# Kernel tuning notes

Hardware: AMD Instinct MI355X
Metric: run time of the kernel (lower is better)

Reference implementation:

```python
import jax, jax.numpy as jnp
import numpy as np

N_R = 100_000   # real nodes
N_E = 1_200_000 # r2r edges
G = 4096        # graphs (= interaction nodes, one per graph)
H = 64          # hidden_dim
ND = 64         # node_dim
ED = 16         # edge_dim
L = 4           # conv_layers
TGT = 1         # target_dim
SLOPE = 0.1     # LeakyReLU negative slope used by ISATconv


def _seg_softmax(logits, seg, n):
    m = jax.ops.segment_max(logits, seg, num_segments=n)
    ex = jnp.exp(logits - m[seg])
    s = jax.ops.segment_sum(ex, seg, num_segments=n)
    return ex / s[seg]


def setup_inputs() -> dict:
    key = jax.random.key(0)
    ks = jax.random.split(key, 20)
    inp = {}
    inp['r_node'] = jax.random.normal(ks[0], (N_R, ND), jnp.float32)
    inp['i_node'] = jax.random.normal(ks[1], (G, 1), jnp.float32)
    inp['r_edge'] = jax.random.normal(ks[2], (N_E, ED), jnp.float32)
    inp['d_edge'] = jax.random.uniform(ks[3], (N_R, 1), jnp.float32)
    inp['r2r_src'] = jax.random.randint(ks[4], (N_E,), 0, N_R, jnp.int32)
    inp['r2r_dst'] = jax.random.randint(ks[5], (N_E,), 0, N_R, jnp.int32)
    inp['graph_id'] = jnp.sort(jax.random.randint(ks[6], (N_R,), 0, G, jnp.int32))
    sc = 1.0 / np.sqrt(H)
    inp['W_r'] = jax.random.normal(ks[7], (ND, H), jnp.float32) * (1.0 / np.sqrt(ND))
    inp['W_i'] = jax.random.normal(ks[8], (1, H), jnp.float32)
    inp['W_e'] = jax.random.normal(ks[9], (ED, H), jnp.float32) * (1.0 / np.sqrt(ED))
    inp['Wm'] = jax.random.normal(ks[10], (L, H, H), jnp.float32) * sc
    inp['a_s'] = jax.random.normal(ks[11], (L, H), jnp.float32) * sc
    inp['a_d'] = jax.random.normal(ks[12], (L, H), jnp.float32) * sc
    inp['a_e'] = jax.random.normal(ks[13], (L, H), jnp.float32) * sc
    inp['w_d'] = jax.random.normal(ks[14], (1,), jnp.float32)
    inp['b_d'] = jnp.zeros((1,), jnp.float32)
    inp['W_mlp'] = jax.random.normal(ks[15], (3, H, H), jnp.float32) * sc
    inp['b_mlp'] = jnp.zeros((3, H), jnp.float32)
    inp['W_out'] = jax.random.normal(ks[16], (H, TGT), jnp.float32) * sc
    inp['b_out'] = jnp.zeros((TGT,), jnp.float32)
    return inp


def reference(r_node, i_node, r_edge, d_edge, r2r_src, r2r_dst, graph_id,
              W_r, W_i, W_e, Wm, a_s, a_d, a_e, w_d, b_d,
              W_mlp, b_mlp, W_out, b_out):
    lrelu = lambda x: jax.nn.leaky_relu(x, SLOPE)
    n = r_node.shape[0]
    g = i_node.shape[0]
    # embeddings (bias-free linears)
    h = r_node @ W_r          # [N,H]
    hi = i_node @ W_i         # [G,H]
    e = r_edge @ W_e          # [E,H]
    score = None
    # ISAT attention conv layers (gather-compute-scatter), residual
    for l in range(L):
        logits = lrelu(h[r2r_src] @ a_s[l] + h[r2r_dst] @ a_d[l] + e @ a_e[l])  # [E]
        attn = _seg_softmax(logits, r2r_dst, n)
        msg = attn[:, None] * (h[r2r_src] + e)
        agg = jax.ops.segment_sum(msg, r2r_dst, num_segments=n) @ Wm[l]
        h = lrelu(h + agg)
        score = attn
    # interaction-node (d2d) mixing: gate by d_edge, gather to i-nodes, broadcast back
    gate = jax.nn.sigmoid(d_edge * w_d + b_d)                 # [N,1]
    hi = hi + jax.ops.segment_sum(gate * h, graph_id, num_segments=g)
    h = h + gate * hi[graph_id]
    # sum pooling over real-node subgraph per graph
    pooled = jax.ops.segment_sum(h, graph_id, num_segments=g)  # [G,H]
    # MLP readout: 3 hidden ReLU layers + linear output
    x = pooled
    for i in range(3):
        x = jax.nn.relu(x @ W_mlp[i] + b_mlp[i])
    return x @ W_out + b_out
```

## Files before the change

### kernel.cpp

```cpp
#include <hip/hip_runtime.h>
#include <math.h>

#define N_RN 100000
#define N_ED 1200000
#define N_G  4096
#define SCAN_CH 256
#define SCAN_NB ((N_RN + SCAN_CH - 1) / SCAN_CH)

__device__ __forceinline__ float lrelu(float x) { return x > 0.f ? x : 0.1f * x; }

__global__ void k_embed_h(const float* __restrict__ r_node,
                          const float* __restrict__ W_r,
                          const float* __restrict__ a_s0,
                          const float* __restrict__ a_d0,
                          float* __restrict__ h,
                          float* __restrict__ hs, float* __restrict__ hd) {
    __shared__ float Wl[64 * 64];
    __shared__ float arow[4][64];
    int tid = threadIdx.x;
    for (int i = tid; i < 4096; i += 256) Wl[i] = W_r[i];
    __syncthreads();
    int lane = tid & 63, w = tid >> 6;
    float asj = a_s0[lane], adj = a_d0[lane];
    int wid = blockIdx.x * 4 + w;
    int nw = gridDim.x * 4;
    for (int n = wid; n < N_RN; n += nw) {
        arow[w][lane] = r_node[(size_t)n * 64 + lane];
        float acc = 0.f;
#pragma unroll
        for (int d4 = 0; d4 < 16; ++d4) {
            float4 a = *(const float4*)&arow[w][d4 * 4];
            int d = d4 * 4;
            acc += a.x * Wl[(d + 0) * 64 + lane];
            acc += a.y * Wl[(d + 1) * 64 + lane];
            acc += a.z * Wl[(d + 2) * 64 + lane];
            acc += a.w * Wl[(d + 3) * 64 + lane];
        }
        h[(size_t)n * 64 + lane] = acc;
        float x = acc * asj, y = acc * adj;
#pragma unroll
        for (int off = 32; off; off >>= 1) {
            x += __shfl_xor(x, off, 64);
            y += __shfl_xor(y, off, 64);
        }
        if (lane == 0) { hs[n] = x; hd[n] = y; }
    }
}

__global__ void k_wewm(const float* __restrict__ W_e,
                       const float* __restrict__ Wm,
                       const float* __restrict__ a_e,
                       float* __restrict__ WeWm,
                       float* __restrict__ was_all) {
    int idx = blockIdx.x * blockDim.x + threadIdx.x;
    if (idx < 4096) {
        int l = idx >> 10, rem = idx & 1023;
        int t = rem >> 6, j = rem & 63;
        float acc = 0.f;
        for (int d = 0; d < 64; ++d)
            acc += W_e[t * 64 + d] * Wm[l * 4096 + d * 64 + j];
        WeWm[idx] = acc;
    } else {
        int r = idx - 4096;
        if (r < 64) {
            int l = r >> 4, t = r & 15;
            float acc = 0.f;
            for (int j = 0; j < 64; ++j)
                acc += W_e[t * 64 + j] * a_e[l * 64 + j];
            was_all[r] = acc;
        }
    }
}

__global__ void k_hist(const int* __restrict__ dst, int* __restrict__ deg) {
    int k = blockIdx.x * blockDim.x + threadIdx.x;
    if (k < N_ED) atomicAdd(deg + dst[k], 1);
}

__global__ void k_scan_a(const int* __restrict__ deg, int* __restrict__ bsum) {
    __shared__ int lds[SCAN_CH];
    int b = blockIdx.x, t = threadIdx.x;
    int i = b * SCAN_CH + t;
    int v = (i < N_RN) ? deg[i] : 0;
    lds[t] = v;
    __syncthreads();
    for (int d = 128; d; d >>= 1) {
        if (t < d) lds[t] += lds[t + d];
        __syncthreads();
    }
    if (t == 0) bsum[b] = lds[0];
}

__global__ void k_scan_b(int* __restrict__ bsum) {
    __shared__ int lds[512];
    int t = threadIdx.x;
    int v = (t < SCAN_NB) ? bsum[t] : 0;
    lds[t] = v;
    __syncthreads();
    for (int d = 1; d < 512; d <<= 1) {
        int u = (t >= d) ? lds[t - d] : 0;
        __syncthreads();
        lds[t] += u;
        __syncthreads();
    }
    if (t < SCAN_NB) bsum[t] = lds[t] - v;
}

__global__ void k_scan_c(const int* __restrict__ deg, const int* __restrict__ bsum,
                         int* __restrict__ off, int* __restrict__ cur) {
    __shared__ int lds[SCAN_CH];
    int b = blockIdx.x, t = threadIdx.x;
    int i = b * SCAN_CH + t;
    int v = (i < N_RN) ? deg[i] : 0;
    lds[t] = v;
    __syncthreads();
    for (int d = 1; d < SCAN_CH; d <<= 1) {
        int u = (t >= d) ? lds[t - d] : 0;
        __syncthreads();
        lds[t] += u;
        __syncthreads();
    }
    if (i < N_RN) {
        int incl = bsum[b] + lds[t];
        off[i + 1] = incl;
        cur[i] = incl - v;
        if (i == 0) off[0] = 0;
    }
}

__global__ void k_scatter_idx(const int* __restrict__ dst,
                              int* __restrict__ cur,
                              int* __restrict__ eperm) {
    int k = blockIdx.x * blockDim.x + threadIdx.x;
    if (k >= N_ED) return;
    int pos = atomicAdd(cur + dst[k], 1);
    eperm[pos] = k;
}

__global__ void k_permute(const int* __restrict__ eperm,
                          const int* __restrict__ src,
                          const float* __restrict__ r_edge,
                          const float* __restrict__ was_all,
                          int2* __restrict__ se,
                          float* __restrict__ r16_perm) {
    int pos = blockIdx.x * blockDim.x + threadIdx.x;
    if (pos >= N_ED) return;
    int k = eperm[pos];
    int sk = src[k];
    const float4* row = (const float4*)(r_edge + (size_t)k * 16);
    float4 r0 = row[0], r1 = row[1], r2 = row[2], r3 = row[3];
    float4* o = (float4*)(r16_perm + (size_t)pos * 16);
    o[0] = r0; o[1] = r1; o[2] = r2; o[3] = r3;
#pragma unroll
    for (int l = 0; l < 4; ++l) {
        const float* wa = was_all + l * 16;
        float e = r0.x * wa[0] + r0.y * wa[1] + r0.z * wa[2] + r0.w * wa[3]
                + r1.x * wa[4] + r1.y * wa[5] + r1.z * wa[6] + r1.w * wa[7]
                + r2.x * wa[8] + r2.y * wa[9] + r2.z * wa[10] + r2.w * wa[11]
                + r3.x * wa[12] + r3.y * wa[13] + r3.z * wa[14] + r3.w * wa[15];
        se[(size_t)l * N_ED + pos] = make_int2(sk, __float_as_int(e));
    }
}

__global__ void k_layer(const float* __restrict__ h_in,
                        const float* __restrict__ hs, const float* __restrict__ hd,
                        const int* __restrict__ off,
                        const int2* __restrict__ se_l,
                        const float* __restrict__ r16_perm,
                        const float* __restrict__ Wm_l,
                        const float* __restrict__ WeWm_l,
                        const float* __restrict__ a_s_n, const float* __restrict__ a_d_n,
                        float* __restrict__ h_out,
                        float* __restrict__ hs_out, float* __restrict__ hd_out) {
    __shared__ float Wl[4096];
    __shared__ float Ww[1024];
    __shared__ float arow[8][4 * 68 + 4];
    int tid = threadIdx.x;
    for (int i = tid; i < 4096; i += 512) Wl[i] = Wm_l[i];
    for (int i = tid; i < 1024; i += 512) Ww[i] = WeWm_l[i];
    __syncthreads();
    int lane = tid & 63, w = tid >> 6;
    int g = lane >> 4, lg = lane & 15;
    float4 as4 = *(const float4*)&a_s_n[lg << 2];
    float4 ad4 = *(const float4*)&a_d_n[lg << 2];
    const int SENT = __float_as_int(-1e38f);
    int Wv = blockIdx.x * 8 + w;
    int NW = gridDim.x * 8;
    for (int nb = Wv * 4; nb < N_RN; nb += NW * 4) {
        int n = nb + g;
        bool nact = n < N_RN;
        int base = 0, end = 0;
        if (nact) { base = off[n]; end = off[n + 1]; }
        float hdn = nact ? hd[n] : 0.f;
        float m = -1e38f, s = 0.f, racc = 0.f;
        float ax = 0.f, ay = 0.f, az = 0.f, aw = 0.f;
        int nch = (end - base + 15) >> 4;
        int nmax = nch;
        nmax = max(nmax, __shfl_xor(nmax, 16, 64));
        nmax = max(nmax, __shfl_xor(nmax, 32, 64));
        int2 v = make_int2(0, SENT);
        if (lg < end - base) v = se_l[base + lg];
        float hsv = hs[v.x];
        for (int c = 0; c < nmax; ++c) {
            int cb = base + (c << 4);
            int rem = end - cb;
            int cnt = rem > 16 ? 16 : (rem > 0 ? rem : 0);
            int2 vn = make_int2(0, SENT);
            int cbn = cb + 16;
            if (lg < end - cbn) vn = se_l[cbn + lg];
            float ep = __int_as_float(v.y);
            float lgt = lrelu(hsv + hdn + ep);
            float cm = lgt;
            cm = fmaxf(cm, __shfl_xor(cm, 1, 16));
            cm = fmaxf(cm, __shfl_xor(cm, 2, 16));
            cm = fmaxf(cm, __shfl_xor(cm, 4, 16));
            cm = fmaxf(cm, __shfl_xor(cm, 8, 16));
            float newm = fmaxf(m, cm);
            float scale = (m > -1e37f) ? __expf(m - newm) : 0.f;
            s *= scale; racc *= scale;
            ax *= scale; ay *= scale; az *= scale; aw *= scale;
            m = newm;
            float wvv = __expf(lgt - m);
            s += wvv;
            int sk = v.x;
            float hsn = hs[vn.x];
            const float* hb = h_in;
            int e = 0;
            for (; e + 3 < cnt; e += 4) {
                float w0 = __shfl(wvv, e, 16);
                float w1 = __shfl(wvv, e + 1, 16);
                float w2 = __shfl(wvv, e + 2, 16);
                float w3 = __shfl(wvv, e + 3, 16);
                int   s0 = __shfl(sk, e, 16);
                int   s1 = __shfl(sk, e + 1, 16);
                int   s2 = __shfl(sk, e + 2, 16);
                int   s3 = __shfl(sk, e + 3, 16);
                const float4 h0v = *(const float4*)(hb + (size_t)s0 * 64 + (lg << 2));
                const float4 h1v = *(const float4*)(hb + (size_t)s1 * 64 + (lg << 2));
                const float4 h2v = *(const float4*)(hb + (size_t)s2 * 64 + (lg << 2));
                const float4 h3v = *(const float4*)(hb + (size_t)s3 * 64 + (lg << 2));
                float q0 = r16_perm[(size_t)(cb + e) * 16 + lg];
                float q1 = r16_perm[(size_t)(cb + e + 1) * 16 + lg];
                float q2 = r16_perm[(size_t)(cb + e + 2) * 16 + lg];
                float q3 = r16_perm[(size_t)(cb + e + 3) * 16 + lg];
                ax += w0 * h0v.x + w1 * h1v.x + w2 * h2v.x + w3 * h3v.x;
                ay += w0 * h0v.y + w1 * h1v.y + w2 * h2v.y + w3 * h3v.y;
                az += w0 * h0v.z + w1 * h1v.z + w2 * h2v.z + w3 * h3v.z;
                aw += w0 * h0v.w + w1 * h1v.w + w2 * h2v.w + w3 * h3v.w;
                racc += w0 * q0 + w1 * q1 + w2 * q2 + w3 * q3;
            }
            for (; e < cnt; ++e) {
                float w0 = __shfl(wvv, e, 16);
                int   s0 = __shfl(sk, e, 16);
                const float4 h0v = *(const float4*)(hb + (size_t)s0 * 64 + (lg << 2));
                float q0 = r16_perm[(size_t)(cb + e) * 16 + lg];
                ax += w0 * h0v.x; ay += w0 * h0v.y;
                az += w0 * h0v.z; aw += w0 * h0v.w;
                racc += w0 * q0;
            }
            v = vn; hsv = hsn;
        }
        s += __shfl_xor(s, 1, 16);
        s += __shfl_xor(s, 2, 16);
        s += __shfl_xor(s, 4, 16);
        s += __shfl_xor(s, 8, 16);
        float inv = (end > base) ? 1.f / s : 0.f;
        float* ar = &arow[w][g * 68];
        *(float4*)&ar[lg << 2] = make_float4(ax * inv, ay * inv, az * inv, aw * inv);
        float mx = 0.f, my = 0.f, mz = 0.f, mw = 0.f;
#pragma unroll
        for (int d4 = 0; d4 < 16; ++d4) {
            float4 a = *(const float4*)&ar[d4 << 2];
            const float* wl = &Wl[(d4 << 2) * 64 + (lg << 2)];
            float4 w0 = *(const float4*)&wl[0];
            float4 w1 = *(const float4*)&wl[64];
            float4 w2 = *(const float4*)&wl[128];
            float4 w3 = *(const float4*)&wl[192];
            mx += a.x * w0.x + a.y * w1.x + a.z * w2.x + a.w * w3.x;
            my += a.x * w0.y + a.y * w1.y + a.z * w2.y + a.w * w3.y;
            mz += a.x * w0.z + a.y * w1.z + a.z * w2.z + a.w * w3.z;
            mw += a.x * w0.w + a.y * w1.w + a.z * w2.w + a.w * w3.w;
        }
        float rs = racc * inv;
#pragma unroll
        for (int t = 0; t < 16; ++t) {
            float rt = __shfl(rs, t, 16);
            const float4 wt = *(const float4*)&Ww[t * 64 + (lg << 2)];
            mx += rt * wt.x; my += rt * wt.y; mz += rt * wt.z; mw += rt * wt.w;
        }
        if (nact) {
            const float4 hi4 = *(const float4*)(h_in + (size_t)n * 64 + (lg << 2));
            float4 hv;
            hv.x = lrelu(hi4.x + mx); hv.y = lrelu(hi4.y + my);
            hv.z = lrelu(hi4.z + mz); hv.w = lrelu(hi4.w + mw);
            *(float4*)(h_out + (size_t)n * 64 + (lg << 2)) = hv;
            float x = hv.x * as4.x + hv.y * as4.y + hv.z * as4.z + hv.w * as4.w;
            float y = hv.x * ad4.x + hv.y * ad4.y + hv.z * ad4.z + hv.w * ad4.w;
            x += __shfl_xor(x, 1, 16); x += __shfl_xor(x, 2, 16);
            x += __shfl_xor(x, 4, 16); x += __shfl_xor(x, 8, 16);
            y += __shfl_xor(y, 1, 16); y += __shfl_xor(y, 2, 16);
            y += __shfl_xor(y, 4, 16); y += __shfl_xor(y, 8, 16);
            if (lg == 0) { hs_out[n] = x; hd_out[n] = y; }
        }
    }
}

__global__ void k_readout(const float* __restrict__ h,
                          const float* __restrict__ d_edge,
                          const int* __restrict__ graph_id,
                          const float* __restrict__ i_node,
                          const float* __restrict__ W_i,
                          const float* __restrict__ w_d,
                          const float* __restrict__ b_d,
                          const float* __restrict__ W_mlp,
                          const float* __restrict__ b_mlp,
                          const float* __restrict__ W_out,
                          const float* __restrict__ b_out,
                          float* __restrict__ out) {
    int g = blockIdx.x, j = threadIdx.x;
    int lo = 0, hi = N_RN;
    while (lo < hi) { int mid = (lo + hi) >> 1; if (graph_id[mid] < g) lo = mid + 1; else hi = mid; }
    int start = lo;
    hi = N_RN;
    while (lo < hi) { int mid = (lo + hi) >> 1; if (graph_id[mid] < g + 1) lo = mid + 1; else hi = mid; }
    int end = lo;

    float wd = w_d[0], bd = b_d[0];
    float acc0 = 0.f, acc1 = 0.f, sg = 0.f;
    for (int n = start; n < end; ++n) {
        float hv = h[(size_t)n * 64 + j];
        float de = d_edge[n];
        float gate = 1.f / (1.f + __expf(-(de * wd + bd)));
        acc0 += hv;
        acc1 += gate * hv;
        sg += gate;
    }
    float hij = i_node[g] * W_i[j] + acc1;
    float pooled = acc0 + sg * hij;

    __shared__ float xa[64], xb[64];
    xa[j] = pooled;
    __syncthreads();
#pragma unroll
    for (int layer = 0; layer < 3; ++layer) {
        const float* W = W_mlp + layer * 4096;
        float* srcb = (layer & 1) ? xb : xa;
        float* dstb = (layer & 1) ? xa : xb;
        float acc = b_mlp[layer * 64 + j];
        for (int d = 0; d < 64; ++d) acc += srcb[d] * W[d * 64 + j];
        acc = fmaxf(acc, 0.f);
        __syncthreads();
        dstb[j] = acc;
        __syncthreads();
    }
    float v = xb[j] * W_out[j];
#pragma unroll
    for (int off = 32; off; off >>= 1) v += __shfl_xor(v, off, 64);
    if (j == 0) out[g] = v + b_out[0];
}

extern "C" void kernel_launch(void* const* d_in, const int* in_sizes, int n_in,
                              void* d_out, int out_size, void* d_ws, size_t ws_size,
                              hipStream_t stream) {
    const float* r_node  = (const float*)d_in[0];
    const float* i_node  = (const float*)d_in[1];
    const float* r_edge  = (const float*)d_in[2];
    const float* d_edge  = (const float*)d_in[3];
    const int*   r2r_src = (const int*)d_in[4];
    const int*   r2r_dst = (const int*)d_in[5];
    const int*   graph_id= (const int*)d_in[6];
    const float* W_r     = (const float*)d_in[7];
    const float* W_i     = (const float*)d_in[8];
    const float* W_e     = (const float*)d_in[9];
    const float* Wm      = (const float*)d_in[10];
    const float* a_s     = (const float*)d_in[11];
    const float* a_d     = (const float*)d_in[12];
    const float* a_e     = (const float*)d_in[13];
    const float* w_d     = (const float*)d_in[14];
    const float* b_d     = (const float*)d_in[15];
    const float* W_mlp   = (const float*)d_in[16];
    const float* b_mlp   = (const float*)d_in[17];
    const float* W_out   = (const float*)d_in[18];
    const float* b_out   = (const float*)d_in[19];
    float* out = (float*)d_out;

    float* ws = (float*)d_ws;
    float* h0   = ws;
    float* h1   = h0 + (size_t)N_RN * 64;
    float* hs0  = h1 + (size_t)N_RN * 64;
    float* hd0  = hs0 + N_RN;
    float* hs1  = hd0 + N_RN;
    float* hd1  = hs1 + N_RN;
    float* WeWm = hd1 + N_RN;
    float* wasb = WeWm + 4096;
    int*   deg  = (int*)(wasb + 64);
    int*   offs = deg + N_RN;
    int*   cur  = offs + N_RN + 1;
    int*   bsum = cur + N_RN;
    int*   eperm= bsum + 512;
    int2*  se   = (int2*)(eperm + N_ED);
    float* r16_perm = (float*)(se + (size_t)4 * N_ED);

    k_wewm<<<17, 256, 0, stream>>>(W_e, Wm, a_e, WeWm, wasb);
    hipMemsetAsync(deg, 0, N_RN * sizeof(int), stream);
    k_hist<<<(N_ED + 255) / 256, 256, 0, stream>>>(r2r_dst, deg);
    k_scan_a<<<SCAN_NB, SCAN_CH, 0, stream>>>(deg, bsum);
    k_scan_b<<<1, 512, 0, stream>>>(bsum);
    k_scan_c<<<SCAN_NB, SCAN_CH, 0, stream>>>(deg, bsum, offs, cur);
    k_scatter_idx<<<(N_ED + 255) / 256, 256, 0, stream>>>(r2r_dst, cur, eperm);
    k_permute<<<(N_ED + 255) / 256, 256, 0, stream>>>(eperm, r2r_src, r_edge, wasb,
                                                      se, r16_perm);

    k_embed_h<<<2048, 256, 0, stream>>>(r_node, W_r, a_s, a_d, h0, hs0, hd0);

    float* hin = h0;  float* hout = h1;
    float* hsi = hs0; float* hdi = hd0;
    float* hso = hs1; float* hdo = hd1;
    for (int l = 0; l < 4; ++l) {
        int ln = (l + 1) & 3;
        k_layer<<<1024, 512, 0, stream>>>(hin, hsi, hdi, offs,
                                          se + (size_t)l * N_ED, r16_perm,
                                          Wm + l * 4096, WeWm + l * 1024,
                                          a_s + ln * 64, a_d + ln * 64,
                                          hout, hso, hdo);
        float* t;
        t = hin; hin = hout; hout = t;
        t = hsi; hsi = hso; hso = t;
        t = hdi; hdi = hdo; hdo = t;
    }

    k_readout<<<N_G, 64, 0, stream>>>(hin, d_edge, graph_id, i_node, W_i, w_d, b_d,
                                      W_mlp, b_mlp, W_out, b_out, out);
}
```

Measured before the change: 776.8 us.

## Store gathered node features and edge features in fp16; record histogram ranks for CSR scatter

Layers now gather neighbour features from an fp16 copy of h and read permuted edge features stored as fp16. This halves the bytes of the random gathers in each layer, while residual and output math stays in fp32. The CSR build also records each edge's atomic rank during the histogram, so the scatter step computes its position without a second atomic pass. This costs an extra rank array and an extra fp16 write per layer, and adds fp16 rounding error to the aggregated messages.

```diff
diff --git a/kernel.cpp b/kernel.cpp
--- a/kernel.cpp
+++ b/kernel.cpp
@@ -1,4 +1,5 @@
 #include <hip/hip_runtime.h>
+#include <hip/hip_fp16.h>
 #include <math.h>
 
 #define N_RN 100000
@@ -14,6 +15,7 @@
                           const float* __restrict__ a_s0,
                           const float* __restrict__ a_d0,
                           float* __restrict__ h,
+                          __half* __restrict__ h16,
                           float* __restrict__ hs, float* __restrict__ hd) {
     __shared__ float Wl[64 * 64];
     __shared__ float arow[4][64];
@@ -37,6 +39,7 @@
             acc += a.w * Wl[(d + 3) * 64 + lane];
         }
         h[(size_t)n * 64 + lane] = acc;
+        h16[(size_t)n * 64 + lane] = __float2half(acc);
         float x = acc * asj, y = acc * adj;
 #pragma unroll
         for (int off = 32; off; off >>= 1) {
@@ -72,9 +75,10 @@
     }
 }
 
-__global__ void k_hist(const int* __restrict__ dst, int* __restrict__ deg) {
+__global__ void k_hist(const int* __restrict__ dst, int* __restrict__ deg,
+                       int* __restrict__ rank) {
     int k = blockIdx.x * blockDim.x + threadIdx.x;
-    if (k < N_ED) atomicAdd(deg + dst[k], 1);
+    if (k < N_ED) rank[k] = atomicAdd(deg + dst[k], 1);
 }
 
 __global__ void k_scan_a(const int* __restrict__ deg, int* __restrict__ bsum) {
@@ -107,7 +111,7 @@
 }
 
 __global__ void k_scan_c(const int* __restrict__ deg, const int* __restrict__ bsum,
-                         int* __restrict__ off, int* __restrict__ cur) {
+                         int* __restrict__ off) {
     __shared__ int lds[SCAN_CH];
     int b = blockIdx.x, t = threadIdx.x;
     int i = b * SCAN_CH + t;
@@ -121,20 +125,21 @@
         __syncthreads();
     }
     if (i < N_RN) {
-        int incl = bsum[b] + lds[t];
-        off[i + 1] = incl;
-        cur[i] = incl - v;
+        off[i + 1] = bsum[b] + lds[t];
         if (i == 0) off[0] = 0;
     }
 }
 
 __global__ void k_scatter_idx(const int* __restrict__ dst,
-                              int* __restrict__ cur,
+                              const int* __restrict__ rank,
+                              const int* __restrict__ off,
                               int* __restrict__ eperm) {
-    int k = blockIdx.x * blockDim.x + threadIdx.x;
-    if (k >= N_ED) return;
-    int pos = atomicAdd(cur + dst[k], 1);
-    eperm[pos] = k;
+    int tid = blockIdx.x * blockDim.x + threadIdx.x;
+    int nt = gridDim.x * blockDim.x;
+    for (int k = tid; k < N_ED; k += nt) {
+        int pos = off[dst[k]] + rank[k];
+        __builtin_nontemporal_store(k, eperm + pos);
+    }
 }
 
 __global__ void k_permute(const int* __restrict__ eperm,
@@ -142,15 +147,20 @@
                           const float* __restrict__ r_edge,
                           const float* __restrict__ was_all,
                           int2* __restrict__ se,
-                          float* __restrict__ r16_perm) {
+                          __half* __restrict__ r16h) {
     int pos = blockIdx.x * blockDim.x + threadIdx.x;
     if (pos >= N_ED) return;
     int k = eperm[pos];
     int sk = src[k];
     const float4* row = (const float4*)(r_edge + (size_t)k * 16);
     float4 r0 = row[0], r1 = row[1], r2 = row[2], r3 = row[3];
-    float4* o = (float4*)(r16_perm + (size_t)pos * 16);
-    o[0] = r0; o[1] = r1; o[2] = r2; o[3] = r3;
+    __half2 p0 = __floats2half2_rn(r0.x, r0.y), p1 = __floats2half2_rn(r0.z, r0.w);
+    __half2 p2 = __floats2half2_rn(r1.x, r1.y), p3 = __floats2half2_rn(r1.z, r1.w);
+    __half2 p4 = __floats2half2_rn(r2.x, r2.y), p5 = __floats2half2_rn(r2.z, r2.w);
+    __half2 p6 = __floats2half2_rn(r3.x, r3.y), p7 = __floats2half2_rn(r3.z, r3.w);
+    uint4* o = (uint4*)(r16h + (size_t)pos * 16);
+    o[0] = make_uint4(*(unsigned*)&p0, *(unsigned*)&p1, *(unsigned*)&p2, *(unsigned*)&p3);
+    o[1] = make_uint4(*(unsigned*)&p4, *(unsigned*)&p5, *(unsigned*)&p6, *(unsigned*)&p7);
 #pragma unroll
     for (int l = 0; l < 4; ++l) {
         const float* wa = was_all + l * 16;
@@ -163,14 +173,16 @@
 }
 
 __global__ void k_layer(const float* __restrict__ h_in,
+                        const __half* __restrict__ h16_in,
                         const float* __restrict__ hs, const float* __restrict__ hd,
                         const int* __restrict__ off,
                         const int2* __restrict__ se_l,
-                        const float* __restrict__ r16_perm,
+                        const __half* __restrict__ r16h,
                         const float* __restrict__ Wm_l,
                         const float* __restrict__ WeWm_l,
                         const float* __restrict__ a_s_n, const float* __restrict__ a_d_n,
                         float* __restrict__ h_out,
+                        __half* __restrict__ h16_out,
                         float* __restrict__ hs_out, float* __restrict__ hd_out) {
     __shared__ float Wl[4096];
     __shared__ float Ww[1024];
@@ -224,7 +236,6 @@
             s += wvv;
             int sk = v.x;
             float hsn = hs[vn.x];
-            const float* hb = h_in;
             int e = 0;
             for (; e + 3 < cnt; e += 4) {
                 float w0 = __shfl(wvv, e, 16);
@@ -235,27 +246,37 @@
                 int   s1 = __shfl(sk, e + 1, 16);
                 int   s2 = __shfl(sk, e + 2, 16);
                 int   s3 = __shfl(sk, e + 3, 16);
-                const float4 h0v = *(const float4*)(hb + (size_t)s0 * 64 + (lg << 2));
-                const float4 h1v = *(const float4*)(hb + (size_t)s1 * 64 + (lg << 2));
-                const float4 h2v = *(const float4*)(hb + (size_t)s2 * 64 + (lg << 2));
-                const float4 h3v = *(const float4*)(hb + (size_t)s3 * 64 + (lg << 2));
-                float q0 = r16_perm[(size_t)(cb + e) * 16 + lg];
-                float q1 = r16_perm[(size_t)(cb + e + 1) * 16 + lg];
-                float q2 = r16_perm[(size_t)(cb + e + 2) * 16 + lg];
-                float q3 = r16_perm[(size_t)(cb + e + 3) * 16 + lg];
-                ax += w0 * h0v.x + w1 * h1v.x + w2 * h2v.x + w3 * h3v.x;
-                ay += w0 * h0v.y + w1 * h1v.y + w2 * h2v.y + w3 * h3v.y;
-                az += w0 * h0v.z + w1 * h1v.z + w2 * h2v.z + w3 * h3v.z;
-                aw += w0 * h0v.w + w1 * h1v.w + w2 * h2v.w + w3 * h3v.w;
+                uint2 hp0 = *(const uint2*)(h16_in + (size_t)s0 * 64 + (lg << 2));
+                uint2 hp1 = *(const uint2*)(h16_in + (size_t)s1 * 64 + (lg << 2));
+                uint2 hp2 = *(const uint2*)(h16_in + (size_t)s2 * 64 + (lg << 2));
+                uint2 hp3 = *(const uint2*)(h16_in + (size_t)s3 * 64 + (lg << 2));
+                float q0 = __half2float(r16h[(size_t)(cb + e) * 16 + lg]);
+                float q1 = __half2float(r16h[(size_t)(cb + e + 1) * 16 + lg]);
+                float q2 = __half2float(r16h[(size_t)(cb + e + 2) * 16 + lg]);
+                float q3 = __half2float(r16h[(size_t)(cb + e + 3) * 16 + lg]);
+                float2 a0 = __half22float2(*(__half2*)&hp0.x);
+                float2 b0 = __half22float2(*(__half2*)&hp0.y);
+                float2 a1 = __half22float2(*(__half2*)&hp1.x);
+                float2 b1 = __half22float2(*(__half2*)&hp1.y);
+                float2 a2 = __half22float2(*(__half2*)&hp2.x);
+                float2 b2 = __half22float2(*(__half2*)&hp2.y);
+                float2 a3 = __half22float2(*(__half2*)&hp3.x);
+                float2 b3 = __half22float2(*(__half2*)&hp3.y);
+                ax += w0 * a0.x + w1 * a1.x + w2 * a2.x + w3 * a3.x;
+                ay += w0 * a0.y + w1 * a1.y + w2 * a2.y + w3 * a3.y;
+                az += w0 * b0.x + w1 * b1.x + w2 * b2.x + w3 * b3.x;
+                aw += w0 * b0.y + w1 * b1.y + w2 * b2.y + w3 * b3.y;
                 racc += w0 * q0 + w1 * q1 + w2 * q2 + w3 * q3;
             }
             for (; e < cnt; ++e) {
                 float w0 = __shfl(wvv, e, 16);
                 int   s0 = __shfl(sk, e, 16);
-                const float4 h0v = *(const float4*)(hb + (size_t)s0 * 64 + (lg << 2));
-                float q0 = r16_perm[(size_t)(cb + e) * 16 + lg];
-                ax += w0 * h0v.x; ay += w0 * h0v.y;
-                az += w0 * h0v.z; aw += w0 * h0v.w;
+                uint2 hp0 = *(const uint2*)(h16_in + (size_t)s0 * 64 + (lg << 2));
+                float q0 = __half2float(r16h[(size_t)(cb + e) * 16 + lg]);
+                float2 a0 = __half22float2(*(__half2*)&hp0.x);
+                float2 b0 = __half22float2(*(__half2*)&hp0.y);
+                ax += w0 * a0.x; ay += w0 * a0.y;
+                az += w0 * b0.x; aw += w0 * b0.y;
                 racc += w0 * q0;
             }
             v = vn; hsv = hsn;
@@ -294,6 +315,10 @@
             hv.x = lrelu(hi4.x + mx); hv.y = lrelu(hi4.y + my);
             hv.z = lrelu(hi4.z + mz); hv.w = lrelu(hi4.w + mw);
             *(float4*)(h_out + (size_t)n * 64 + (lg << 2)) = hv;
+            __half2 p0 = __floats2half2_rn(hv.x, hv.y);
+            __half2 p1 = __floats2half2_rn(hv.z, hv.w);
+            *(uint2*)(h16_out + (size_t)n * 64 + (lg << 2)) =
+                make_uint2(*(unsigned*)&p0, *(unsigned*)&p1);
             float x = hv.x * as4.x + hv.y * as4.y + hv.z * as4.z + hv.w * as4.w;
             float y = hv.x * ad4.x + hv.y * ad4.y + hv.z * ad4.z + hv.w * ad4.w;
             x += __shfl_xor(x, 1, 16); x += __shfl_xor(x, 2, 16);
@@ -395,38 +420,42 @@
     float* wasb = WeWm + 4096;
     int*   deg  = (int*)(wasb + 64);
     int*   offs = deg + N_RN;
-    int*   cur  = offs + N_RN + 1;
-    int*   bsum = cur + N_RN;
+    int*   rank = offs + N_RN + 1;
+    int*   bsum = rank + N_ED;
     int*   eperm= bsum + 512;
     int2*  se   = (int2*)(eperm + N_ED);
-    float* r16_perm = (float*)(se + (size_t)4 * N_ED);
+    __half* r16h = (__half*)(se + (size_t)4 * N_ED);
+    __half* h16a = r16h + (size_t)N_ED * 16;
+    __half* h16b = h16a + (size_t)N_RN * 64;
 
     k_wewm<<<17, 256, 0, stream>>>(W_e, Wm, a_e, WeWm, wasb);
     hipMemsetAsync(deg, 0, N_RN * sizeof(int), stream);
-    k_hist<<<(N_ED + 255) / 256, 256, 0, stream>>>(r2r_dst, deg);
+    k_hist<<<(N_ED + 255) / 256, 256, 0, stream>>>(r2r_dst, deg, rank);
     k_scan_a<<<SCAN_NB, SCAN_CH, 0, stream>>>(deg, bsum);
     k_scan_b<<<1, 512, 0, stream>>>(bsum);
-    k_scan_c<<<SCAN_NB, SCAN_CH, 0, stream>>>(deg, bsum, offs, cur);
-    k_scatter_idx<<<(N_ED + 255) / 256, 256, 0, stream>>>(r2r_dst, cur, eperm);
+    k_scan_c<<<SCAN_NB, SCAN_CH, 0, stream>>>(deg, bsum, offs);
+    k_scatter_idx<<<1172, 256, 0, stream>>>(r2r_dst, rank, offs, eperm);
     k_permute<<<(N_ED + 255) / 256, 256, 0, stream>>>(eperm, r2r_src, r_edge, wasb,
-                                                      se, r16_perm);
-
-    k_embed_h<<<2048, 256, 0, stream>>>(r_node, W_r, a_s, a_d, h0, hs0, hd0);
+                                                      se, r16h);
+
+    k_embed_h<<<2048, 256, 0, stream>>>(r_node, W_r, a_s, a_d, h0, h16a, hs0, hd0);
 
     float* hin = h0;  float* hout = h1;
+    __half* h16i = h16a; __half* h16o = h16b;
     float* hsi = hs0; float* hdi = hd0;
     float* hso = hs1; float* hdo = hd1;
     for (int l = 0; l < 4; ++l) {
         int ln = (l + 1) & 3;
-        k_layer<<<1024, 512, 0, stream>>>(hin, hsi, hdi, offs,
-                                          se + (size_t)l * N_ED, r16_perm,
+        k_layer<<<1024, 512, 0, stream>>>(hin, h16i, hsi, hdi, offs,
+                                          se + (size_t)l * N_ED, r16h,
                                           Wm + l * 4096, WeWm + l * 1024,
                                           a_s + ln * 64, a_d + ln * 64,
-                                          hout, hso, hdo);
+                                          hout, h16o, hso, hdo);
         float* t;
         t = hin; hin = hout; hout = t;
         t = hsi; hsi = hso; hso = t;
         t = hdi; hdi = hdo; hdo = t;
+        __half* th = h16i; h16i = h16o; h16o = th;
     }
 
     k_readout<<<N_G, 64, 0, stream>>>(hin, d_edge, graph_id, i_node, W_i, w_d, b_d,
```

Result: faster. 711.9 us (-8.4%).
